# Optimization experiments

Measured on AMD Instinct MI355X. Metric: run time of the kernel, lower is better.

## Reference

```python
import jax, jax.numpy as jnp
from jax import lax
import numpy as np

B, H, W, C = 8, 56, 56, 384
NUM_HEADS, HEAD_CH = 6, 64
BN_EPS = 1e-5
DN = ('NHWC', 'HWIO', 'NHWC')


def conv_proj(x, dw_kernel, bn_scale, bn_bias, bn_mean, bn_var, pw_kernel, stride):
    """Depthwise conv -> BatchNorm (eval) -> 1x1 pointwise conv, all SAME padding."""
    in_ch = x.shape[-1]
    x = lax.conv_general_dilated(x, dw_kernel, (stride, stride), 'SAME',
                                 dimension_numbers=DN, feature_group_count=in_ch)
    x = (x - bn_mean) * (bn_scale / jnp.sqrt(bn_var + BN_EPS)) + bn_bias
    x = lax.conv_general_dilated(x, pw_kernel, (1, 1), 'SAME', dimension_numbers=DN)
    return x


def setup_inputs() -> dict:
    key = jax.random.key(0)
    ks = jax.random.split(key, 16)
    d = {
        'inputs_q': jax.random.normal(ks[0], (B, H, W, C), jnp.float32),
        'inputs_kv': jax.random.normal(ks[1], (B, H, W, C), jnp.float32),
        'out_kernel': jax.random.normal(ks[2], (NUM_HEADS, HEAD_CH, C), jnp.float32) * 0.05,
    }
    for i, p in enumerate(['q', 'k', 'v']):
        d[f'{p}_dw_kernel'] = jax.random.normal(ks[3 + i], (3, 3, 1, C), jnp.float32) * 0.1
        d[f'{p}_bn_scale'] = jnp.ones((C,), jnp.float32)
        d[f'{p}_bn_bias'] = jnp.zeros((C,), jnp.float32)
        d[f'{p}_bn_mean'] = jnp.zeros((C,), jnp.float32)
        d[f'{p}_bn_var'] = jnp.ones((C,), jnp.float32)
        d[f'{p}_pw_kernel'] = jax.random.normal(ks[6 + i], (1, 1, C, NUM_HEADS * HEAD_CH), jnp.float32) * 0.05
    return d


def reference(inputs_q, inputs_kv,
              q_dw_kernel, q_bn_scale, q_bn_bias, q_bn_mean, q_bn_var, q_pw_kernel,
              k_dw_kernel, k_bn_scale, k_bn_bias, k_bn_mean, k_bn_var, k_pw_kernel,
              v_dw_kernel, v_bn_scale, v_bn_bias, v_bn_mean, v_bn_var, v_pw_kernel,
              out_kernel):
    q = conv_proj(inputs_q, q_dw_kernel, q_bn_scale, q_bn_bias, q_bn_mean, q_bn_var, q_pw_kernel, 1)
    k = conv_proj(inputs_kv, k_dw_kernel, k_bn_scale, k_bn_bias, k_bn_mean, k_bn_var, k_pw_kernel, 2)
    v = conv_proj(inputs_kv, v_dw_kernel, v_bn_scale, v_bn_bias, v_bn_mean, v_bn_var, v_pw_kernel, 2)

    def to_tokens(x):  # [b,H,W,h*d] -> [b,HW,h,d]
        b, hh, ww, _ = x.shape
        return x.reshape(b, hh * ww, NUM_HEADS, HEAD_CH)

    q = to_tokens(q) / jnp.sqrt(jnp.float32(HEAD_CH))
    k = to_tokens(k)
    v = to_tokens(v)

    attn = jnp.einsum('bqhd,bkhd->bhqk', q, k)       # [b,h,Nq,Nkv]
    attn = jax.nn.softmax(attn, axis=-1)
    out = jnp.einsum('bhqk,bkhd->bqhd', attn, v)     # [b,Nq,h,d]
    out = jnp.einsum('bqhd,hdo->bqo', out, out_kernel)  # DenseGeneral over (h,d)
    return out
```

## Files before the change

### kernel.cpp

```cpp
#include <hip/hip_runtime.h>
#include <hip/hip_bf16.h>
#include <hip/hip_fp16.h>

#define BB 8
#define HH 56
#define WW 56
#define CC 384
#define NHD 6
#define DD 64
#define HK 28
#define WK 28
#define NQ (HH*WW)
#define NKV (HK*WK)
#define NTOK (BB*NQ)
#define NTOKKV (BB*NKV)
#define BN_EPS 1e-5f
#define LOG2E 1.44269504f

typedef _Float16 f16;
typedef _Float16 f16x2 __attribute__((ext_vector_type(2)));
typedef _Float16 f16x4 __attribute__((ext_vector_type(4)));
typedef _Float16 f16x8 __attribute__((ext_vector_type(8)));
typedef float f32x4 __attribute__((ext_vector_type(4)));

__device__ __forceinline__ float fast_exp2(float x) {
#if __has_builtin(__builtin_amdgcn_exp2f)
  return __builtin_amdgcn_exp2f(x);
#else
  return __expf(x * 0.69314718056f);
#endif
}

__device__ __forceinline__ f16x4 pack4(float p0, float p1, float p2, float p3) {
#if __has_builtin(__builtin_amdgcn_cvt_pkrtz)
  f16x2 a = __builtin_bit_cast(f16x2, __builtin_amdgcn_cvt_pkrtz(p0, p1));
  f16x2 b = __builtin_bit_cast(f16x2, __builtin_amdgcn_cvt_pkrtz(p2, p3));
  return __builtin_shufflevector(a, b, 0, 1, 2, 3);
#else
  f16x4 r; r[0] = (f16)p0; r[1] = (f16)p1; r[2] = (f16)p2; r[3] = (f16)p3;
  return r;
#endif
}

__device__ __forceinline__ void dw_s1_body(
    int blk, int tid, const float* __restrict__ in, const float* __restrict__ w,
    const float* __restrict__ bns, const float* __restrict__ bnb,
    const float* __restrict__ bnm, const float* __restrict__ bnv,
    f16* __restrict__ out) {
  int idx = blk * 256 + tid;
  int pp = idx / 96;
  int c = (idx % 96) * 4;
  int b = pp / (HH * WK);
  int rem = pp % (HH * WK);
  int y = rem / WK, xh = rem % WK;
  int x0 = xh * 2;
  float a0x = 0, a0y = 0, a0z = 0, a0w = 0;
  float a1x = 0, a1y = 0, a1z = 0, a1w = 0;
#pragma unroll
  for (int kh = 0; kh < 3; ++kh) {
    int iy = y + kh - 1;
    if ((unsigned)iy >= (unsigned)HH) continue;
    const float* rp = in + ((size_t)(b * HH + iy) * WW) * CC + c;
    const float4 z4 = {0.f, 0.f, 0.f, 0.f};
    const float4 v0 = (x0 > 0) ? *(const float4*)(rp + (size_t)(x0 - 1) * CC) : z4;
    const float4 v1 = *(const float4*)(rp + (size_t)x0 * CC);
    const float4 v2 = *(const float4*)(rp + (size_t)(x0 + 1) * CC);
    const float4 v3 = (x0 < 54) ? *(const float4*)(rp + (size_t)(x0 + 2) * CC) : z4;
    const float4 w0 = *(const float4*)(w + (kh * 3 + 0) * CC + c);
    const float4 w1 = *(const float4*)(w + (kh * 3 + 1) * CC + c);
    const float4 w2 = *(const float4*)(w + (kh * 3 + 2) * CC + c);
    a0x = fmaf(v0.x, w0.x, fmaf(v1.x, w1.x, fmaf(v2.x, w2.x, a0x)));
    a0y = fmaf(v0.y, w0.y, fmaf(v1.y, w1.y, fmaf(v2.y, w2.y, a0y)));
    a0z = fmaf(v0.z, w0.z, fmaf(v1.z, w1.z, fmaf(v2.z, w2.z, a0z)));
    a0w = fmaf(v0.w, w0.w, fmaf(v1.w, w1.w, fmaf(v2.w, w2.w, a0w)));
    a1x = fmaf(v1.x, w0.x, fmaf(v2.x, w1.x, fmaf(v3.x, w2.x, a1x)));
    a1y = fmaf(v1.y, w0.y, fmaf(v2.y, w1.y, fmaf(v3.y, w2.y, a1y)));
    a1z = fmaf(v1.z, w0.z, fmaf(v2.z, w1.z, fmaf(v3.z, w2.z, a1z)));
    a1w = fmaf(v1.w, w0.w, fmaf(v2.w, w1.w, fmaf(v3.w, w2.w, a1w)));
  }
  const float4 s = *(const float4*)(bns + c);
  const float4 bi = *(const float4*)(bnb + c);
  const float4 m = *(const float4*)(bnm + c);
  const float4 va = *(const float4*)(bnv + c);
  f16x4 r0, r1;
  float g;
  g = s.x * rsqrtf(va.x + BN_EPS); r0[0] = (f16)fmaf(a0x - m.x, g, bi.x); r1[0] = (f16)fmaf(a1x - m.x, g, bi.x);
  g = s.y * rsqrtf(va.y + BN_EPS); r0[1] = (f16)fmaf(a0y - m.y, g, bi.y); r1[1] = (f16)fmaf(a1y - m.y, g, bi.y);
  g = s.z * rsqrtf(va.z + BN_EPS); r0[2] = (f16)fmaf(a0z - m.z, g, bi.z); r1[2] = (f16)fmaf(a1z - m.z, g, bi.z);
  g = s.w * rsqrtf(va.w + BN_EPS); r0[3] = (f16)fmaf(a0w - m.w, g, bi.w); r1[3] = (f16)fmaf(a1w - m.w, g, bi.w);
  const size_t pix0 = (size_t)b * NQ + y * WW + x0;
  *(f16x4*)(out + pix0 * CC + c) = r0;
  *(f16x4*)(out + (pix0 + 1) * CC + c) = r1;
}

__device__ __forceinline__ void dw_s2_body(
    int blk, int tid, const float* __restrict__ in,
    const float* __restrict__ wk_, const float* __restrict__ kbs, const float* __restrict__ kbb,
    const float* __restrict__ kbm, const float* __restrict__ kbv,
    const float* __restrict__ wv_, const float* __restrict__ vbs, const float* __restrict__ vbb,
    const float* __restrict__ vbm, const float* __restrict__ vbv,
    f16* __restrict__ outk, f16* __restrict__ outv) {
  int idx = blk * 256 + tid;
  int pix = idx / 96;
  int c = (idx % 96) * 4;
  int b = pix / (HK * WK);
  int p = pix % (HK * WK);
  int oy = p / WK, ox = p % WK;
  float kx = 0, ky = 0, kz = 0, kw4 = 0;
  float vx = 0, vy = 0, vz = 0, vw4 = 0;
#pragma unroll
  for (int kh = 0; kh < 3; ++kh) {
    int iy = oy * 2 + kh;
    if (iy >= HH) continue;
#pragma unroll
    for (int kwi = 0; kwi < 3; ++kwi) {
      int ix = ox * 2 + kwi;
      if (ix >= WW) continue;
      const float4 v = *(const float4*)(in + (((size_t)(b * HH + iy) * WW + ix) * CC + c));
      const float4 a = *(const float4*)(wk_ + ((kh * 3 + kwi) * CC + c));
      const float4 bq = *(const float4*)(wv_ + ((kh * 3 + kwi) * CC + c));
      kx = fmaf(v.x, a.x, kx); ky = fmaf(v.y, a.y, ky);
      kz = fmaf(v.z, a.z, kz); kw4 = fmaf(v.w, a.w, kw4);
      vx = fmaf(v.x, bq.x, vx); vy = fmaf(v.y, bq.y, vy);
      vz = fmaf(v.z, bq.z, vz); vw4 = fmaf(v.w, bq.w, vw4);
    }
  }
  {
    const float4 s = *(const float4*)(kbs + c);
    const float4 bi = *(const float4*)(kbb + c);
    const float4 m = *(const float4*)(kbm + c);
    const float4 va = *(const float4*)(kbv + c);
    f16x4 r; float g;
    g = s.x * rsqrtf(va.x + BN_EPS); r[0] = (f16)fmaf(kx - m.x, g, bi.x);
    g = s.y * rsqrtf(va.y + BN_EPS); r[1] = (f16)fmaf(ky - m.y, g, bi.y);
    g = s.z * rsqrtf(va.z + BN_EPS); r[2] = (f16)fmaf(kz - m.z, g, bi.z);
    g = s.w * rsqrtf(va.w + BN_EPS); r[3] = (f16)fmaf(kw4 - m.w, g, bi.w);
    *(f16x4*)(outk + (size_t)pix * CC + c) = r;
  }
  {
    const float4 s = *(const float4*)(vbs + c);
    const float4 bi = *(const float4*)(vbb + c);
    const float4 m = *(const float4*)(vbm + c);
    const float4 va = *(const float4*)(vbv + c);
    f16x4 r; float g;
    g = s.x * rsqrtf(va.x + BN_EPS); r[0] = (f16)fmaf(vx - m.x, g, bi.x);
    g = s.y * rsqrtf(va.y + BN_EPS); r[1] = (f16)fmaf(vy - m.y, g, bi.y);
    g = s.z * rsqrtf(va.z + BN_EPS); r[2] = (f16)fmaf(vz - m.z, g, bi.z);
    g = s.w * rsqrtf(va.w + BN_EPS); r[3] = (f16)fmaf(vw4 - m.w, g, bi.w);
    *(f16x4*)(outv + (size_t)pix * CC + c) = r;
  }
}

__global__ __launch_bounds__(256) void preprocess(
    const float* __restrict__ inputs_q, const float* __restrict__ inputs_kv,
    const float* __restrict__ q_dwk, const float* __restrict__ q_bs,
    const float* __restrict__ q_bb, const float* __restrict__ q_bm,
    const float* __restrict__ q_bv,
    const float* __restrict__ k_dwk, const float* __restrict__ k_bs,
    const float* __restrict__ k_bb, const float* __restrict__ k_bm,
    const float* __restrict__ k_bv,
    const float* __restrict__ v_dwk, const float* __restrict__ v_bs,
    const float* __restrict__ v_bb, const float* __restrict__ v_bm,
    const float* __restrict__ v_bv,
    const float* __restrict__ w0, const float* __restrict__ w1,
    const float* __restrict__ w2, const float* __restrict__ w3,
    f16* __restrict__ o0, f16* __restrict__ o1,
    f16* __restrict__ o2, f16* __restrict__ o3,
    f16* __restrict__ qdw, f16* __restrict__ kdw, f16* __restrict__ vdw) {
  __shared__ float t[32][33];
  const int blk = blockIdx.x;
  const int tid = threadIdx.x;
  if (blk < 4704) {
    dw_s1_body(blk, tid, inputs_q, q_dwk, q_bs, q_bb, q_bm, q_bv, qdw);
  } else if (blk < 7056) {
    dw_s2_body(blk - 4704, tid, inputs_kv,
               k_dwk, k_bs, k_bb, k_bm, k_bv,
               v_dwk, v_bs, v_bb, v_bm, v_bv, kdw, vdw);
  } else {
    const int r = blk - 7056;
    const int z = r / 144, rem = r % 144;
    const int bx = rem % 12, by = rem / 12;
    const float* src = z == 0 ? w0 : z == 1 ? w1 : z == 2 ? w2 : w3;
    f16* dst = z == 0 ? o0 : z == 1 ? o1 : z == 2 ? o2 : o3;
    const int k0 = bx * 32, n0 = by * 32;
    const int x = tid & 31, y = tid >> 5;
#pragma unroll
    for (int i = 0; i < 4; ++i) t[y + i * 8][x] = src[(size_t)(k0 + y + i * 8) * 384 + n0 + x];
    __syncthreads();
#pragma unroll
    for (int i = 0; i < 4; ++i)
      dst[(size_t)(n0 + y + i * 8) * 384 + k0 + x] = (f16)t[x][y + i * 8];
  }
}

template <int MODE>
__device__ __forceinline__ void gemm_body(
    const f16* __restrict__ A, const f16* __restrict__ Bt,
    float* __restrict__ Cf, f16* __restrict__ Ch, float scale,
    int row0, int col0) {
  __shared__ f16 As[128 * 64];
  __shared__ f16 Bs[128 * 64];
  const int tid = threadIdx.x;
  const int wave = tid >> 6, lane = tid & 63;
  const int c = lane & 15, g = lane >> 4;
  const int wr = wave >> 1, wc = wave & 1;

  const int s_base = wave * 64 + lane;
  f32x4 acc[4][4] = {};

  for (int k0 = 0; k0 < 384; k0 += 64) {
    __syncthreads();
#pragma unroll
    for (int j = 0; j < 4; ++j) {
      const int s = j * 256 + s_base;
      const int row = s >> 3, sch = s & 7;
      const int lch = sch ^ (row & 7);
      const f16* sa = A + (size_t)(row0 + row) * 384 + k0 + lch * 8;
      __builtin_amdgcn_global_load_lds(
          (const __attribute__((address_space(1))) void*)sa,
          (__attribute__((address_space(3))) void*)(As + j * 2048 + wave * 512), 16, 0, 0);
      const f16* sb = Bt + (size_t)(col0 + row) * 384 + k0 + lch * 8;
      __builtin_amdgcn_global_load_lds(
          (const __attribute__((address_space(1))) void*)sb,
          (__attribute__((address_space(3))) void*)(Bs + j * 2048 + wave * 512), 16, 0, 0);
    }
    __syncthreads();

#pragma unroll
    for (int kh = 0; kh < 2; ++kh) {
      f16x8 bf[4];
#pragma unroll
      for (int n = 0; n < 4; ++n) {
        const int row = wc * 64 + n * 16 + c;
        bf[n] = *(const f16x8*)(Bs + (size_t)row * 64 + ((kh * 4 + g) ^ (row & 7)) * 8);
      }
#pragma unroll
      for (int m = 0; m < 4; ++m) {
        const int row = wr * 64 + m * 16 + c;
        f16x8 af = *(const f16x8*)(As + (size_t)row * 64 + ((kh * 4 + g) ^ (row & 7)) * 8);
#pragma unroll
        for (int n = 0; n < 4; ++n)
          acc[m][n] = __builtin_amdgcn_mfma_f32_16x16x32_f16(af, bf[n], acc[m][n], 0, 0, 0);
      }
    }
  }

  if (MODE == 2) {
#pragma unroll
    for (int m = 0; m < 4; ++m)
#pragma unroll
      for (int n = 0; n < 4; ++n) {
        const int gr = row0 + wr * 64 + m * 16 + g * 4;
        const int col = col0 + wc * 64 + n * 16 + c;
        const int bb = gr / NKV;
        const int kv = gr - bb * NKV;
        f16x4 pk;
#pragma unroll
        for (int r = 0; r < 4; ++r) pk[r] = (f16)(acc[m][n][r] * scale);
        *(f16x4*)(Ch + ((size_t)bb * 384 + col) * NKV + kv) = pk;
      }
  } else {
#pragma unroll
    for (int m = 0; m < 4; ++m)
#pragma unroll
      for (int n = 0; n < 4; ++n)
#pragma unroll
        for (int r = 0; r < 4; ++r) {
          const size_t row = row0 + wr * 64 + m * 16 + g * 4 + r;
          const size_t col = col0 + wc * 64 + n * 16 + c;
          if (MODE == 1) Ch[row * 384 + col] = (f16)(acc[m][n][r] * scale);
          else           Cf[row * 384 + col] = acc[m][n][r] * scale;
        }
  }
}

__global__ __launch_bounds__(256) void gemm_qkv(
    const f16* __restrict__ qdw, const f16* __restrict__ wqt, f16* __restrict__ qf, float qscale,
    const f16* __restrict__ kdw, const f16* __restrict__ wkt, f16* __restrict__ kf,
    const f16* __restrict__ vdw, const f16* __restrict__ wvt, f16* __restrict__ vtp) {
  const int blk = blockIdx.x;
  if (blk < 588) {
    gemm_body<1>(qdw, wqt, nullptr, qf, qscale, (blk % 196) * 128, (blk / 196) * 128);
  } else if (blk < 735) {
    const int r = blk - 588;
    gemm_body<1>(kdw, wkt, nullptr, kf, 1.0f, (r % 49) * 128, (r / 49) * 128);
  } else {
    const int r = blk - 735;
    gemm_body<2>(vdw, wvt, nullptr, vtp, 1.0f, (r % 49) * 128, (r / 49) * 128);
  }
}

template <int MODE>
__global__ __launch_bounds__(256) void gemm_mfma(
    const f16* __restrict__ A, const f16* __restrict__ Bt,
    float* __restrict__ Cf, f16* __restrict__ Ch, float scale) {
  gemm_body<MODE>(A, Bt, Cf, Ch, scale, blockIdx.x * 128, blockIdx.y * 128);
}

__global__ __launch_bounds__(256) void attn_mfma(
    const f16* __restrict__ qp, const f16* __restrict__ kp,
    const f16* __restrict__ vt, f16* __restrict__ op) {
  __shared__ f16 Ks[64 * 64];
  __shared__ f16 Vs[64 * 64];
  __shared__ f16 Ps[4][16 * 64];
  const int bid = blockIdx.x;
  const int qt = bid % 49;
  const int bh = bid / 49;
  const int h = bh % NHD, b = bh / NHD;
  const int tid = threadIdx.x;
  const int wave = tid >> 6, lane = tid & 63;
  const int c = lane & 15, g = lane >> 4;

  const size_t qrow = (size_t)b * NQ + qt * 64 + wave * 16 + c;
  f16x8 qa[2];
  qa[0] = *(const f16x8*)(qp + qrow * 384 + h * 64 + g * 8);
  qa[1] = *(const f16x8*)(qp + qrow * 384 + h * 64 + 32 + g * 8);

  f16x8 vones;
#pragma unroll
  for (int j = 0; j < 8; ++j) vones[j] = (f16)1.0f;

  const int tid8 = tid >> 3, tch = tid & 7;
  const int lch = tch ^ (tid8 & 7);

  const f16* kbase = kp + ((size_t)b * NKV) * 384 + h * 64;
  const f16* vbase = vt + ((size_t)(b * 384 + h * 64)) * NKV;

  float mrun = -1e30f;
  f32x4 o[4] = {};
  f32x4 osum = {};
  f16* prow = &Ps[wave][0];

  for (int t0 = 0; t0 < NKV; t0 += 64) {
    __syncthreads();
    {
      int kv0 = t0 + tid8; if (kv0 > NKV - 1) kv0 = NKV - 1;
      int kv1 = t0 + 32 + tid8; if (kv1 > NKV - 1) kv1 = NKV - 1;
      __builtin_amdgcn_global_load_lds(
          (const __attribute__((address_space(1))) void*)(kbase + (size_t)kv0 * 384 + lch * 8),
          (__attribute__((address_space(3))) void*)(Ks + wave * 512), 16, 0, 0);
      __builtin_amdgcn_global_load_lds(
          (const __attribute__((address_space(1))) void*)(kbase + (size_t)kv1 * 384 + lch * 8),
          (__attribute__((address_space(3))) void*)(Ks + 2048 + wave * 512), 16, 0, 0);
      int col = t0 + lch * 8; if (col > NKV - 8) col = NKV - 8;
      __builtin_amdgcn_global_load_lds(
          (const __attribute__((address_space(1))) void*)(vbase + (size_t)tid8 * NKV + col),
          (__attribute__((address_space(3))) void*)(Vs + wave * 512), 16, 0, 0);
      __builtin_amdgcn_global_load_lds(
          (const __attribute__((address_space(1))) void*)(vbase + (size_t)(32 + tid8) * NKV + col),
          (__attribute__((address_space(3))) void*)(Vs + 2048 + wave * 512), 16, 0, 0);
    }
    __syncthreads();

    f32x4 s[4] = {};
    __builtin_amdgcn_s_setprio(1);
#pragma unroll
    for (int kh = 0; kh < 2; ++kh) {
#pragma unroll
      for (int ct = 0; ct < 4; ++ct) {
        const int row = ct * 16 + c;
        const int sch = (kh * 4 + g) ^ (row & 7);
        f16x8 kb = *(const f16x8*)(Ks + row * 64 + sch * 8);
        s[ct] = __builtin_amdgcn_mfma_f32_16x16x32_f16(kb, qa[kh], s[ct], 0, 0, 0);
      }
    }
    __builtin_amdgcn_s_setprio(0);
    if (t0 + 64 > NKV) {
#pragma unroll
      for (int ct = 0; ct < 4; ++ct)
#pragma unroll
        for (int r = 0; r < 4; ++r)
          if (t0 + ct * 16 + g * 4 + r >= NKV) s[ct][r] = -1e30f;
    }

    float mt = s[0][0];
#pragma unroll
    for (int ct = 0; ct < 4; ++ct)
#pragma unroll
      for (int r = 0; r < 4; ++r) mt = fmaxf(mt, s[ct][r]);
    mt = fmaxf(mt, __shfl_xor(mt, 16));
    mt = fmaxf(mt, __shfl_xor(mt, 32));

    if (__ballot(mt > mrun + 8.0f)) {
      const float mnew = fmaxf(mrun, mt);
      const float corr = fast_exp2(mrun - mnew);
      mrun = mnew;
#pragma unroll
      for (int r = 0; r < 4; ++r) {
        const float co = __shfl(corr, g * 4 + r);
#pragma unroll
        for (int dt = 0; dt < 4; ++dt) o[dt][r] *= co;
        osum[r] *= co;
      }
    }

#pragma unroll
    for (int ct = 0; ct < 4; ++ct) {
      const float p0 = fast_exp2(s[ct][0] - mrun);
      const float p1 = fast_exp2(s[ct][1] - mrun);
      const float p2 = fast_exp2(s[ct][2] - mrun);
      const float p3 = fast_exp2(s[ct][3] - mrun);
      const int sch = (ct * 2 + (g >> 1)) ^ (c & 7);
      *(f16x4*)(prow + c * 64 + sch * 8 + (g & 1) * 4) = pack4(p0, p1, p2, p3);
    }

    __builtin_amdgcn_s_setprio(1);
#pragma unroll
    for (int ks = 0; ks < 2; ++ks) {
      const int sp = (ks * 4 + g) ^ (c & 7);
      f16x8 pa = *(const f16x8*)(prow + c * 64 + sp * 8);
#pragma unroll
      for (int dt = 0; dt < 4; ++dt) {
        const int d = dt * 16 + c;
        f16x8 vb = *(const f16x8*)(Vs + d * 64 + sp * 8);
        o[dt] = __builtin_amdgcn_mfma_f32_16x16x32_f16(pa, vb, o[dt], 0, 0, 0);
      }
      osum = __builtin_amdgcn_mfma_f32_16x16x32_f16(pa, vones, osum, 0, 0, 0);
    }
    __builtin_amdgcn_s_setprio(0);
  }

  f16* obase = op + ((size_t)(b * NQ + qt * 64 + wave * 16)) * 384 + h * 64;
#pragma unroll
  for (int r = 0; r < 4; ++r) {
    const float iv = 1.0f / osum[r];
#pragma unroll
    for (int dt = 0; dt < 4; ++dt)
      obase[(size_t)(g * 4 + r) * 384 + dt * 16 + c] = (f16)(o[dt][r] * iv);
  }
}

extern "C" void kernel_launch(void* const* d_in, const int* in_sizes, int n_in,
                              void* d_out, int out_size, void* d_ws, size_t ws_size,
                              hipStream_t stream) {
  const float* inputs_q  = (const float*)d_in[0];
  const float* inputs_kv = (const float*)d_in[1];
  const float* out_kern  = (const float*)d_in[2];
  const float* q_dwk = (const float*)d_in[3];
  const float* q_bs  = (const float*)d_in[4];
  const float* q_bb  = (const float*)d_in[5];
  const float* q_bm  = (const float*)d_in[6];
  const float* q_bv  = (const float*)d_in[7];
  const float* q_pwk = (const float*)d_in[8];
  const float* k_dwk = (const float*)d_in[9];
  const float* k_bs  = (const float*)d_in[10];
  const float* k_bb  = (const float*)d_in[11];
  const float* k_bm  = (const float*)d_in[12];
  const float* k_bv  = (const float*)d_in[13];
  const float* k_pwk = (const float*)d_in[14];
  const float* v_dwk = (const float*)d_in[15];
  const float* v_bs  = (const float*)d_in[16];
  const float* v_bb  = (const float*)d_in[17];
  const float* v_bm  = (const float*)d_in[18];
  const float* v_bv  = (const float*)d_in[19];
  const float* v_pwk = (const float*)d_in[20];

  char* wsb = (char*)d_ws;
  f16* qdw = (f16*)(wsb + 0);
  f16* kdw = (f16*)(wsb + 19267584);
  f16* vdw = (f16*)(wsb + 24084480);
  f16* qf  = (f16*)(wsb + 28901376);
  f16* kf  = (f16*)(wsb + 48168960);
  f16* vtp = (f16*)(wsb + 57802752);
  f16* of  = (f16*)(wsb + 62619648);
  f16* wqt = (f16*)(wsb + 81887232);
  f16* wkt = (f16*)(wsb + 82182144);
  f16* wvt = (f16*)(wsb + 82477056);
  f16* wot = (f16*)(wsb + 82771968);

  preprocess<<<7632, 256, 0, stream>>>(
      inputs_q, inputs_kv,
      q_dwk, q_bs, q_bb, q_bm, q_bv,
      k_dwk, k_bs, k_bb, k_bm, k_bv,
      v_dwk, v_bs, v_bb, v_bm, v_bv,
      q_pwk, k_pwk, v_pwk, out_kern, wqt, wkt, wvt, wot,
      qdw, kdw, vdw);
  gemm_qkv<<<882, 256, 0, stream>>>(qdw, wqt, qf, 0.125f * LOG2E,
                                    kdw, wkt, kf, vdw, wvt, vtp);
  attn_mfma<<<BB * NHD * 49, 256, 0, stream>>>(qf, kf, vtp, of);
  gemm_mfma<0><<<dim3(196, 3), 256, 0, stream>>>(of, wot, (float*)d_out, nullptr, 1.0f);
}
```

Baseline: 153.7 us.

## Stage 128-token KV tiles per sync and remap attention blocks across XCDs

The attention kernel now loads 128 KV tokens of K and V into LDS per iteration instead of 64. It then processes them as two 64-token halves, which halves the number of block-wide barriers and load phases. The V tile uses a 16-chunk XOR swizzle to fit the wider row. Block IDs are also remapped so consecutive blocks on the same XCD work on the same batch/head and can share L2 for K/V. The cost is doubled LDS use for K/V, which may reduce occupancy.

```diff
diff --git a/kernel.cpp b/kernel.cpp
--- a/kernel.cpp
+++ b/kernel.cpp
@@ -297,15 +297,17 @@
   gemm_body<MODE>(A, Bt, Cf, Ch, scale, blockIdx.x * 128, blockIdx.y * 128);
 }
 
+#define KVSTEP 128
 __global__ __launch_bounds__(256) void attn_mfma(
     const f16* __restrict__ qp, const f16* __restrict__ kp,
     const f16* __restrict__ vt, f16* __restrict__ op) {
-  __shared__ f16 Ks[64 * 64];
-  __shared__ f16 Vs[64 * 64];
+  __shared__ f16 Ks[KVSTEP * 64];
+  __shared__ f16 Vs[64 * KVSTEP];
   __shared__ f16 Ps[4][16 * 64];
-  const int bid = blockIdx.x;
-  const int qt = bid % 49;
-  const int bh = bid / 49;
+  const int bid0 = blockIdx.x;
+  const int lb = (bid0 & 7) * 294 + (bid0 >> 3);
+  const int qt = lb % 49;
+  const int bh = lb / 49;
   const int h = bh % NHD, b = bh / NHD;
   const int tid = threadIdx.x;
   const int wave = tid >> 6, lane = tid & 63;
@@ -320,9 +322,6 @@
 #pragma unroll
   for (int j = 0; j < 8; ++j) vones[j] = (f16)1.0f;
 
-  const int tid8 = tid >> 3, tch = tid & 7;
-  const int lch = tch ^ (tid8 & 7);
-
   const f16* kbase = kp + ((size_t)b * NKV) * 384 + h * 64;
   const f16* vbase = vt + ((size_t)(b * 384 + h * 64)) * NKV;
 
@@ -331,93 +330,100 @@
   f32x4 osum = {};
   f16* prow = &Ps[wave][0];
 
-  for (int t0 = 0; t0 < NKV; t0 += 64) {
+  for (int st = 0; st < 7; ++st) {
+    const int t0 = st * KVSTEP;
     __syncthreads();
     {
-      int kv0 = t0 + tid8; if (kv0 > NKV - 1) kv0 = NKV - 1;
-      int kv1 = t0 + 32 + tid8; if (kv1 > NKV - 1) kv1 = NKV - 1;
-      __builtin_amdgcn_global_load_lds(
-          (const __attribute__((address_space(1))) void*)(kbase + (size_t)kv0 * 384 + lch * 8),
-          (__attribute__((address_space(3))) void*)(Ks + wave * 512), 16, 0, 0);
-      __builtin_amdgcn_global_load_lds(
-          (const __attribute__((address_space(1))) void*)(kbase + (size_t)kv1 * 384 + lch * 8),
-          (__attribute__((address_space(3))) void*)(Ks + 2048 + wave * 512), 16, 0, 0);
-      int col = t0 + lch * 8; if (col > NKV - 8) col = NKV - 8;
-      __builtin_amdgcn_global_load_lds(
-          (const __attribute__((address_space(1))) void*)(vbase + (size_t)tid8 * NKV + col),
-          (__attribute__((address_space(3))) void*)(Vs + wave * 512), 16, 0, 0);
-      __builtin_amdgcn_global_load_lds(
-          (const __attribute__((address_space(1))) void*)(vbase + (size_t)(32 + tid8) * NKV + col),
-          (__attribute__((address_space(3))) void*)(Vs + 2048 + wave * 512), 16, 0, 0);
+#pragma unroll
+      for (int j = 0; j < 4; ++j) {
+        const int sk = j * 256 + tid;
+        const int kvr = sk >> 3, skc = sk & 7;
+        int krow = t0 + kvr; if (krow > NKV - 1) krow = NKV - 1;
+        __builtin_amdgcn_global_load_lds(
+            (const __attribute__((address_space(1))) void*)(kbase + (size_t)krow * 384 + ((skc ^ (kvr & 7)) * 8)),
+            (__attribute__((address_space(3))) void*)(Ks + j * 2048 + wave * 512), 16, 0, 0);
+        const int dr = sk >> 4, svc = sk & 15;
+        int col = t0 + (svc ^ (dr & 15)) * 8; if (col > NKV - 8) col = NKV - 8;
+        __builtin_amdgcn_global_load_lds(
+            (const __attribute__((address_space(1))) void*)(vbase + (size_t)dr * NKV + col),
+            (__attribute__((address_space(3))) void*)(Vs + j * 2048 + wave * 512), 16, 0, 0);
+      }
     }
     __syncthreads();
 
-    f32x4 s[4] = {};
-    __builtin_amdgcn_s_setprio(1);
-#pragma unroll
-    for (int kh = 0; kh < 2; ++kh) {
+#pragma unroll
+    for (int half = 0; half < 2; ++half) {
+      const int tt = t0 + half * 64;
+      if (tt >= NKV) continue;
+
+      f32x4 s[4] = {};
+      __builtin_amdgcn_s_setprio(1);
+#pragma unroll
+      for (int kh = 0; kh < 2; ++kh) {
+#pragma unroll
+        for (int ct = 0; ct < 4; ++ct) {
+          const int row = half * 64 + ct * 16 + c;
+          const int sch = (kh * 4 + g) ^ (row & 7);
+          f16x8 kb = *(const f16x8*)(Ks + row * 64 + sch * 8);
+          s[ct] = __builtin_amdgcn_mfma_f32_16x16x32_f16(kb, qa[kh], s[ct], 0, 0, 0);
+        }
+      }
+      __builtin_amdgcn_s_setprio(0);
+      if (tt + 64 > NKV) {
+#pragma unroll
+        for (int ct = 0; ct < 4; ++ct)
+#pragma unroll
+          for (int r = 0; r < 4; ++r)
+            if (tt + ct * 16 + g * 4 + r >= NKV) s[ct][r] = -1e30f;
+      }
+
+      float mt = s[0][0];
+#pragma unroll
+      for (int ct = 0; ct < 4; ++ct)
+#pragma unroll
+        for (int r = 0; r < 4; ++r) mt = fmaxf(mt, s[ct][r]);
+      mt = fmaxf(mt, __shfl_xor(mt, 16));
+      mt = fmaxf(mt, __shfl_xor(mt, 32));
+
+      if (__ballot(mt > mrun + 8.0f)) {
+        const float mnew = fmaxf(mrun, mt);
+        const float corr = fast_exp2(mrun - mnew);
+        mrun = mnew;
+#pragma unroll
+        for (int r = 0; r < 4; ++r) {
+          const float co = __shfl(corr, g * 4 + r);
+#pragma unroll
+          for (int dt = 0; dt < 4; ++dt) o[dt][r] *= co;
+          osum[r] *= co;
+        }
+      }
+
 #pragma unroll
       for (int ct = 0; ct < 4; ++ct) {
-        const int row = ct * 16 + c;
-        const int sch = (kh * 4 + g) ^ (row & 7);
-        f16x8 kb = *(const f16x8*)(Ks + row * 64 + sch * 8);
-        s[ct] = __builtin_amdgcn_mfma_f32_16x16x32_f16(kb, qa[kh], s[ct], 0, 0, 0);
-      }
+        const float p0 = fast_exp2(s[ct][0] - mrun);
+        const float p1 = fast_exp2(s[ct][1] - mrun);
+        const float p2 = fast_exp2(s[ct][2] - mrun);
+        const float p3 = fast_exp2(s[ct][3] - mrun);
+        const int sch = (ct * 2 + (g >> 1)) ^ (c & 7);
+        *(f16x4*)(prow + c * 64 + sch * 8 + (g & 1) * 4) = pack4(p0, p1, p2, p3);
+      }
+
+      __builtin_amdgcn_s_setprio(1);
+#pragma unroll
+      for (int ks = 0; ks < 2; ++ks) {
+        const int sp = (ks * 4 + g) ^ (c & 7);
+        f16x8 pa = *(const f16x8*)(prow + c * 64 + sp * 8);
+#pragma unroll
+        for (int dt = 0; dt < 4; ++dt) {
+          const int d = dt * 16 + c;
+          const int cidx = (half * 8 + ks * 4 + g) ^ (d & 15);
+          f16x8 vb = *(const f16x8*)(Vs + (size_t)d * KVSTEP + cidx * 8);
+          o[dt] = __builtin_amdgcn_mfma_f32_16x16x32_f16(pa, vb, o[dt], 0, 0, 0);
+        }
+        osum = __builtin_amdgcn_mfma_f32_16x16x32_f16(pa, vones, osum, 0, 0, 0);
+      }
+      __builtin_amdgcn_s_setprio(0);
     }
-    __builtin_amdgcn_s_setprio(0);
-    if (t0 + 64 > NKV) {
-#pragma unroll
-      for (int ct = 0; ct < 4; ++ct)
-#pragma unroll
-        for (int r = 0; r < 4; ++r)
-          if (t0 + ct * 16 + g * 4 + r >= NKV) s[ct][r] = -1e30f;
-    }
-
-    float mt = s[0][0];
-#pragma unroll
-    for (int ct = 0; ct < 4; ++ct)
-#pragma unroll
-      for (int r = 0; r < 4; ++r) mt = fmaxf(mt, s[ct][r]);
-    mt = fmaxf(mt, __shfl_xor(mt, 16));
-    mt = fmaxf(mt, __shfl_xor(mt, 32));
-
-    if (__ballot(mt > mrun + 8.0f)) {
-      const float mnew = fmaxf(mrun, mt);
-      const float corr = fast_exp2(mrun - mnew);
-      mrun = mnew;
-#pragma unroll
-      for (int r = 0; r < 4; ++r) {
-        const float co = __shfl(corr, g * 4 + r);
-#pragma unroll
-        for (int dt = 0; dt < 4; ++dt) o[dt][r] *= co;
-        osum[r] *= co;
-      }
-    }
-
-#pragma unroll
-    for (int ct = 0; ct < 4; ++ct) {
-      const float p0 = fast_exp2(s[ct][0] - mrun);
-      const float p1 = fast_exp2(s[ct][1] - mrun);
-      const float p2 = fast_exp2(s[ct][2] - mrun);
-      const float p3 = fast_exp2(s[ct][3] - mrun);
-      const int sch = (ct * 2 + (g >> 1)) ^ (c & 7);
-      *(f16x4*)(prow + c * 64 + sch * 8 + (g & 1) * 4) = pack4(p0, p1, p2, p3);
-    }
-
-    __builtin_amdgcn_s_setprio(1);
-#pragma unroll
-    for (int ks = 0; ks < 2; ++ks) {
-      const int sp = (ks * 4 + g) ^ (c & 7);
-      f16x8 pa = *(const f16x8*)(prow + c * 64 + sp * 8);
-#pragma unroll
-      for (int dt = 0; dt < 4; ++dt) {
-        const int d = dt * 16 + c;
-        f16x8 vb = *(const f16x8*)(Vs + d * 64 + sp * 8);
-        o[dt] = __builtin_amdgcn_mfma_f32_16x16x32_f16(pa, vb, o[dt], 0, 0, 0);
-      }
-      osum = __builtin_amdgcn_mfma_f32_16x16x32_f16(pa, vones, osum, 0, 0, 0);
-    }
-    __builtin_amdgcn_s_setprio(0);
   }
 
   f16* obase = op + ((size_t)(b * NQ + qt * 64 + wave * 16)) * 384 + h * 64;
```

New measurement: 153.6 us. No clear change (-0.1%).
